# Kernel optimization log

Measured on AMD Instinct MI355X. Metric: run time of the kernel, lower is better.

Reference implementation:

```python
import jax, jax.numpy as jnp
import numpy as np

N = 16                      # input_dim (state dimension)
EPS = 1e-6
TRIL_R, TRIL_C = np.tril_indices(N)   # 136 lower-triangular slots


def setup_inputs() -> dict:
    key = jax.random.key(0)
    ks = jax.random.split(key, 7)
    B = 131072
    def xavier(k, fan_in, fan_out):
        lim = float(np.sqrt(6.0 / (fan_in + fan_out)))
        return jax.random.uniform(k, (fan_in, fan_out), jnp.float32, -lim, lim)
    return {
        "points": jax.random.normal(ks[0], (B, N), jnp.float32),
        "W0": xavier(ks[1], N, 512),
        "b0": jax.random.normal(ks[2], (512,), jnp.float32) * 0.01,
        "W1": xavier(ks[3], 512, 512),
        "b1": jax.random.normal(ks[4], (512,), jnp.float32) * 0.01,
        "W2": xavier(ks[5], 512, 136),
        "b2": jax.random.normal(ks[6], (136,), jnp.float32) * 0.01,
    }


def reference(points, W0, b0, W1, b1, W2, b2):
    # MLP: tanh, tanh, identity
    h = jnp.tanh(points @ W0 + b0)
    h = jnp.tanh(h @ W1 + b1)
    net = h @ W2 + b2                         # [B, 136] tril entries
    B = points.shape[0]
    # Batched scatter into lower-triangular matrices M: [B, N, N]
    M = jnp.zeros((B, N, N), points.dtype).at[:, TRIL_R, TRIL_C].set(net)
    # x^T (M M^T) x == ||M^T x||^2
    y = jnp.einsum('bij,bi->bj', M, points)   # (M^T x)_j = sum_i M_ij x_i
    vals = jnp.sum(y * y, axis=-1) + EPS * jnp.sum(points * points, axis=-1)
    return vals.reshape(-1, 1)
```

## Files before the change

### kernel.cpp

```cpp
#include <hip/hip_runtime.h>

typedef __bf16 bf16x4 __attribute__((ext_vector_type(4)));
typedef __bf16 bf16x8 __attribute__((ext_vector_type(8)));
typedef float f32x16 __attribute__((ext_vector_type(16)));

#define W0F_OFF 0
#define W1F_OFF 8192
#define W2F_OFF (8192 + 262144)
#define PREP_TOTAL (8192 + 262144 + 81920)

__global__ void prep_weights(const float* __restrict__ W0,
                             const float* __restrict__ W1,
                             const float* __restrict__ W2,
                             __bf16* __restrict__ ws) {
    int t = blockIdx.x * 256 + threadIdx.x;
    if (t < 8192) {
        int j = t & 7, lane = (t >> 3) & 63, nt = t >> 9;
        int n = nt * 32 + (lane & 31);
        int k = (lane >> 5) * 8 + j;
        ws[W0F_OFF + t] = (__bf16)W0[k * 512 + n];
    } else if (t < 8192 + 262144) {
        int u = t - 8192;
        int j = u & 7, lane = (u >> 3) & 63;
        int x = u >> 9;
        int kk = x & 31, nt = x >> 5;
        int n = nt * 32 + (lane & 31);
        int k = kk * 16 + (lane >> 5) * 8 + j;
        ws[W1F_OFF + u] = (__bf16)W1[k * 512 + n];
    } else if (t < PREP_TOTAL) {
        int v = t - (8192 + 262144);
        int j = v & 7, lane = (v >> 3) & 63;
        int x = v >> 9;
        int kk = x & 31, nt = x >> 5;
        int n = nt * 32 + (lane & 31);
        int k = kk * 16 + (lane >> 5) * 8 + j;
        ws[W2F_OFF + v] = (n < 136) ? (__bf16)W2[k * 136 + n] : (__bf16)0.0f;
    }
}

__device__ __forceinline__ float fast_tanh(float x) {
#if __has_builtin(__builtin_amdgcn_exp2f)
    float e = __builtin_amdgcn_exp2f(x * 2.885390081777926f);
#else
    float e = exp2f(x * 2.885390081777926f);
#endif
    return 1.0f - 2.0f * __builtin_amdgcn_rcpf(e + 1.0f);
}

#define HSTR 520
#define NSTR 140

__global__ __launch_bounds__(512, 2)
void fused_mlp_quad(const float* __restrict__ points,
                    const float* __restrict__ b0,
                    const float* __restrict__ b1,
                    const float* __restrict__ b2,
                    const __bf16* __restrict__ ws,
                    float* __restrict__ out) {
    __shared__ __align__(16) unsigned char lds_raw[66560];
    __bf16* h  = (__bf16*)lds_raw;
    float* net = (float*)lds_raw;

    const __bf16* w0f = ws + W0F_OFF;
    const __bf16* w1f = ws + W1F_OFF;
    const __bf16* w2f = ws + W2F_OFF;

    const int tid = threadIdx.x;
    const int w   = tid >> 6;
    const int l   = tid & 63;
    const int ln  = l & 31;
    const int hi  = l >> 5;
    const int row0 = blockIdx.x * 64;

    const int lofs = l * 8;
    const int ofs16 = (blockIdx.x >> 3) & 15;
    const int ofs8  = (blockIdx.x >> 3) & 7;

    {
        bf16x8 bx[2];
#pragma unroll
        for (int bt = 0; bt < 2; ++bt) {
            const float* src = points + (row0 + bt * 32 + ln) * 16 + hi * 8;
            float4 p0 = ((const float4*)src)[0];
            float4 p1 = ((const float4*)src)[1];
            bf16x8 v;
            v[0] = (__bf16)p0.x; v[1] = (__bf16)p0.y; v[2] = (__bf16)p0.z; v[3] = (__bf16)p0.w;
            v[4] = (__bf16)p1.x; v[5] = (__bf16)p1.y; v[6] = (__bf16)p1.z; v[7] = (__bf16)p1.w;
            bx[bt] = v;
        }
#pragma unroll
        for (int t = 0; t < 2; ++t) {
            const int ntg = w * 2 + t;
            bf16x8 wf = *(const bf16x8*)(w0f + ntg * 512 + lofs);
#pragma unroll
            for (int bt = 0; bt < 2; ++bt) {
                f32x16 acc = {};
                acc = __builtin_amdgcn_mfma_f32_32x32x16_bf16(wf, bx[bt], acc, 0, 0, 0);
#pragma unroll
                for (int rg = 0; rg < 4; ++rg) {
                    const int n0 = ntg * 32 + 8 * rg + 4 * hi;
                    float4 bias = *(const float4*)(b0 + n0);
                    bf16x4 v;
                    v[0] = (__bf16)fast_tanh(acc[4 * rg + 0] + bias.x);
                    v[1] = (__bf16)fast_tanh(acc[4 * rg + 1] + bias.y);
                    v[2] = (__bf16)fast_tanh(acc[4 * rg + 2] + bias.z);
                    v[3] = (__bf16)fast_tanh(acc[4 * rg + 3] + bias.w);
                    *(bf16x4*)(h + (bt * 32 + ln) * HSTR + n0) = v;
                }
            }
        }
    }
    __syncthreads();

    f32x16 acc1[2][2] = {};
    {
        const __bf16* arow0 = h + ln * HSTR + hi * 8;
        const __bf16* arow1 = h + (32 + ln) * HSTR + hi * 8;
        const __bf16* wb0 = w1f + (w * 2 + 0) * 16384 + lofs;
        const __bf16* wb1 = w1f + (w * 2 + 1) * 16384 + lofs;
        for (int ks2 = 0; ks2 < 16; ++ks2) {
            const int ks = (ks2 + ofs16) & 15;
            bf16x8 aa[2][2], bb[2][2];
#pragma unroll
            for (int u = 0; u < 2; ++u) {
                const int kk = ks * 2 + u;
                const int vo = kk * 512;
                aa[u][0] = *(const bf16x8*)(arow0 + kk * 16);
                aa[u][1] = *(const bf16x8*)(arow1 + kk * 16);
                bb[u][0] = *(const bf16x8*)(wb0 + vo);
                bb[u][1] = *(const bf16x8*)(wb1 + vo);
            }
#pragma unroll
            for (int u = 0; u < 2; ++u) {
#pragma unroll
                for (int t = 0; t < 2; ++t) {
                    acc1[0][t] = __builtin_amdgcn_mfma_f32_32x32x16_bf16(bb[u][t], aa[u][0], acc1[0][t], 0, 0, 0);
                    acc1[1][t] = __builtin_amdgcn_mfma_f32_32x32x16_bf16(bb[u][t], aa[u][1], acc1[1][t], 0, 0, 0);
                }
            }
        }
    }
    __syncthreads();
#pragma unroll
    for (int t = 0; t < 2; ++t) {
#pragma unroll
        for (int bt = 0; bt < 2; ++bt) {
#pragma unroll
            for (int rg = 0; rg < 4; ++rg) {
                const int n0 = (w * 2 + t) * 32 + 8 * rg + 4 * hi;
                float4 bias = *(const float4*)(b1 + n0);
                bf16x4 v;
                v[0] = (__bf16)fast_tanh(acc1[bt][t][4 * rg + 0] + bias.x);
                v[1] = (__bf16)fast_tanh(acc1[bt][t][4 * rg + 1] + bias.y);
                v[2] = (__bf16)fast_tanh(acc1[bt][t][4 * rg + 2] + bias.z);
                v[3] = (__bf16)fast_tanh(acc1[bt][t][4 * rg + 3] + bias.w);
                *(bf16x4*)(h + (bt * 32 + ln) * HSTR + n0) = v;
            }
        }
    }
    __syncthreads();

    f32x16 acc2a = {}, acc2e = {};
    const int nt2 = w >> 1;
    const int bt2 = w & 1;
    const bool two = (w < 2);
    {
        const __bf16* arowA = h + (bt2 * 32 + ln) * HSTR + hi * 8;
        const __bf16* arowE = h + ((w & 1) * 32 + ln) * HSTR + hi * 8;
        const __bf16* wbA = w2f + nt2 * 16384 + lofs;
        const __bf16* wbE = w2f + 4 * 16384 + lofs;
        for (int ks2 = 0; ks2 < 8; ++ks2) {
            const int ks = (ks2 + ofs8) & 7;
            bf16x8 aaA[2], wA[2], aaE[2], wE[2];
#pragma unroll
            for (int u = 0; u < 2; ++u) {
                const int kk = ks * 4 + u * 2;
                const int vo = kk * 512;
                aaA[u] = *(const bf16x8*)(arowA + kk * 16);
                wA[u]  = *(const bf16x8*)(wbA + vo);
                if (two) {
                    aaE[u] = *(const bf16x8*)(arowE + kk * 16);
                    wE[u]  = *(const bf16x8*)(wbE + vo);
                }
            }
            bf16x8 aaA2[2], wA2[2], aaE2[2], wE2[2];
#pragma unroll
            for (int u = 0; u < 2; ++u) {
                const int kk = ks * 4 + u * 2 + 1;
                const int vo = kk * 512;
                aaA2[u] = *(const bf16x8*)(arowA + kk * 16);
                wA2[u]  = *(const bf16x8*)(wbA + vo);
                if (two) {
                    aaE2[u] = *(const bf16x8*)(arowE + kk * 16);
                    wE2[u]  = *(const bf16x8*)(wbE + vo);
                }
            }
#pragma unroll
            for (int u = 0; u < 2; ++u) {
                acc2a = __builtin_amdgcn_mfma_f32_32x32x16_bf16(wA[u], aaA[u], acc2a, 0, 0, 0);
                acc2a = __builtin_amdgcn_mfma_f32_32x32x16_bf16(wA2[u], aaA2[u], acc2a, 0, 0, 0);
                if (two) {
                    acc2e = __builtin_amdgcn_mfma_f32_32x32x16_bf16(wE[u], aaE[u], acc2e, 0, 0, 0);
                    acc2e = __builtin_amdgcn_mfma_f32_32x32x16_bf16(wE2[u], aaE2[u], acc2e, 0, 0, 0);
                }
            }
        }
    }
    __syncthreads();
    {
#pragma unroll
        for (int rg = 0; rg < 4; ++rg) {
            const int n0 = nt2 * 32 + 8 * rg + 4 * hi;
            float4 bias = *(const float4*)(b2 + n0);
            float4 v;
            v.x = acc2a[4 * rg + 0] + bias.x;
            v.y = acc2a[4 * rg + 1] + bias.y;
            v.z = acc2a[4 * rg + 2] + bias.z;
            v.w = acc2a[4 * rg + 3] + bias.w;
            *(float4*)(net + (bt2 * 32 + ln) * NSTR + n0) = v;
        }
        if (two) {
            const int n0 = 128 + 4 * hi;
            float4 bias = *(const float4*)(b2 + n0);
            float4 v;
            v.x = acc2e[0] + bias.x;
            v.y = acc2e[1] + bias.y;
            v.z = acc2e[2] + bias.z;
            v.w = acc2e[3] + bias.w;
            *(float4*)(net + ((w & 1) * 32 + ln) * NSTR + n0) = v;
        }
    }
    __syncthreads();

    {
        const int r  = tid >> 3;
        const int jg = tid & 7;
        const float* xp = points + (row0 + r) * 16;
        float xv[16];
#pragma unroll
        for (int i = 0; i < 4; ++i) {
            float4 v = ((const float4*)xp)[i];
            xv[i * 4 + 0] = v.x; xv[i * 4 + 1] = v.y;
            xv[i * 4 + 2] = v.z; xv[i * 4 + 3] = v.w;
        }
        float sumsq = 0.f;
#pragma unroll
        for (int i = 0; i < 16; ++i) sumsq += xv[i] * xv[i];
        float p = 0.f;
#pragma unroll
        for (int jj = 0; jj < 2; ++jj) {
            const int j = jg + jj * 8;
            float y = 0.f;
#pragma unroll
            for (int i = 0; i < 16; ++i) {
                float mv = net[r * NSTR + ((i * (i + 1)) >> 1) + j];
                y += (i >= j) ? mv * xv[i] : 0.f;
            }
            p += y * y;
        }
        p += __shfl_xor(p, 1);
        p += __shfl_xor(p, 2);
        p += __shfl_xor(p, 4);
        if (jg == 0) out[row0 + r] = p + 1e-6f * sumsq;
    }
}

extern "C" void kernel_launch(void* const* d_in, const int* in_sizes, int n_in,
                              void* d_out, int out_size, void* d_ws, size_t ws_size,
                              hipStream_t stream) {
    const float* points = (const float*)d_in[0];
    const float* W0 = (const float*)d_in[1];
    const float* b0 = (const float*)d_in[2];
    const float* W1 = (const float*)d_in[3];
    const float* b1 = (const float*)d_in[4];
    const float* W2 = (const float*)d_in[5];
    const float* b2 = (const float*)d_in[6];
    __bf16* ws = (__bf16*)d_ws;
    float* out = (float*)d_out;

    prep_weights<<<(PREP_TOTAL + 255) / 256, 256, 0, stream>>>(W0, W1, W2, ws);

    const int B = in_sizes[0] / 16;
    fused_mlp_quad<<<B / 64, 512, 0, stream>>>(points, b0, b1, b2, ws, out);
}
```

Before: 188.5 us.

## Fold tanh scale into weights, vectorize weight prep, stagger first-wave blocks

Pre-multiplies W0 and W1 by the tanh exp2 constant during weight conversion, so each tanh drops one multiply (bias is folded with an fma). The prep kernel is rewritten so one wave writes a contiguous 512-element fragment as 16-byte vector stores. The first 512 blocks also sleep for a hash-based random delay so they do not all hit the same memory at once. The staggering adds idle time, and scaling before the bf16 cast changes rounding slightly.

Result: slower. 196.8 us (+4.4%).

```diff
diff --git a/kernel.cpp b/kernel.cpp
--- a/kernel.cpp
+++ b/kernel.cpp
@@ -4,45 +4,37 @@
 typedef __bf16 bf16x8 __attribute__((ext_vector_type(8)));
 typedef float f32x16 __attribute__((ext_vector_type(16)));
 
+#define TC 2.885390081777926f
+
 #define W0F_OFF 0
 #define W1F_OFF 8192
 #define W2F_OFF (8192 + 262144)
-#define PREP_TOTAL (8192 + 262144 + 81920)
 
 __global__ void prep_weights(const float* __restrict__ W0,
                              const float* __restrict__ W1,
                              const float* __restrict__ W2,
                              __bf16* __restrict__ ws) {
-    int t = blockIdx.x * 256 + threadIdx.x;
-    if (t < 8192) {
-        int j = t & 7, lane = (t >> 3) & 63, nt = t >> 9;
-        int n = nt * 32 + (lane & 31);
-        int k = (lane >> 5) * 8 + j;
-        ws[W0F_OFF + t] = (__bf16)W0[k * 512 + n];
-    } else if (t < 8192 + 262144) {
-        int u = t - 8192;
-        int j = u & 7, lane = (u >> 3) & 63;
-        int x = u >> 9;
-        int kk = x & 31, nt = x >> 5;
-        int n = nt * 32 + (lane & 31);
-        int k = kk * 16 + (lane >> 5) * 8 + j;
-        ws[W1F_OFF + u] = (__bf16)W1[k * 512 + n];
-    } else if (t < PREP_TOTAL) {
-        int v = t - (8192 + 262144);
-        int j = v & 7, lane = (v >> 3) & 63;
-        int x = v >> 9;
-        int kk = x & 31, nt = x >> 5;
-        int n = nt * 32 + (lane & 31);
-        int k = kk * 16 + (lane >> 5) * 8 + j;
-        ws[W2F_OFF + v] = (n < 136) ? (__bf16)W2[k * 136 + n] : (__bf16)0.0f;
-    }
-}
-
-__device__ __forceinline__ float fast_tanh(float x) {
+    const int wave = blockIdx.x * 8 + (threadIdx.x >> 6);
+    const int l   = threadIdx.x & 63;
+    const int col = l & 31, kh = l >> 5;
+    const float* src; int nt, kk, S, nlim; float scl;
+    if (wave < 16)       { src = W0; nt = wave; kk = 0;      S = 512; nlim = 512; scl = TC; }
+    else if (wave < 528) { int r = wave - 16;  src = W1; nt = r >> 5; kk = r & 31; S = 512; nlim = 512; scl = TC; }
+    else                 { int r = wave - 528; src = W2; nt = r >> 5; kk = r & 31; S = 136; nlim = 136; scl = 1.0f; }
+    const int n  = nt * 32 + col;
+    const int k0 = kk * 16 + kh * 8;
+    bf16x8 v;
+#pragma unroll
+    for (int j = 0; j < 8; ++j)
+        v[j] = (n < nlim) ? (__bf16)(src[(k0 + j) * S + n] * scl) : (__bf16)0.0f;
+    *(bf16x8*)(ws + wave * 512 + l * 8) = v;
+}
+
+__device__ __forceinline__ float fast_tanh_pre(float y) {
 #if __has_builtin(__builtin_amdgcn_exp2f)
-    float e = __builtin_amdgcn_exp2f(x * 2.885390081777926f);
+    float e = __builtin_amdgcn_exp2f(y);
 #else
-    float e = exp2f(x * 2.885390081777926f);
+    float e = exp2f(y);
 #endif
     return 1.0f - 2.0f * __builtin_amdgcn_rcpf(e + 1.0f);
 }
@@ -61,6 +53,18 @@
     __bf16* h  = (__bf16*)lds_raw;
     float* net = (float*)lds_raw;
 
+    {
+        const unsigned d = (blockIdx.x < 512)
+                         ? ((blockIdx.x * 2654435761u) >> 29) : 0u;
+        if (d > 0) __builtin_amdgcn_s_sleep(64);
+        if (d > 1) __builtin_amdgcn_s_sleep(64);
+        if (d > 2) __builtin_amdgcn_s_sleep(64);
+        if (d > 3) __builtin_amdgcn_s_sleep(64);
+        if (d > 4) __builtin_amdgcn_s_sleep(64);
+        if (d > 5) __builtin_amdgcn_s_sleep(64);
+        if (d > 6) __builtin_amdgcn_s_sleep(64);
+    }
+
     const __bf16* w0f = ws + W0F_OFF;
     const __bf16* w1f = ws + W1F_OFF;
     const __bf16* w2f = ws + W2F_OFF;
@@ -101,10 +105,10 @@
                     const int n0 = ntg * 32 + 8 * rg + 4 * hi;
                     float4 bias = *(const float4*)(b0 + n0);
                     bf16x4 v;
-                    v[0] = (__bf16)fast_tanh(acc[4 * rg + 0] + bias.x);
-                    v[1] = (__bf16)fast_tanh(acc[4 * rg + 1] + bias.y);
-                    v[2] = (__bf16)fast_tanh(acc[4 * rg + 2] + bias.z);
-                    v[3] = (__bf16)fast_tanh(acc[4 * rg + 3] + bias.w);
+                    v[0] = (__bf16)fast_tanh_pre(fmaf(TC, bias.x, acc[4 * rg + 0]));
+                    v[1] = (__bf16)fast_tanh_pre(fmaf(TC, bias.y, acc[4 * rg + 1]));
+                    v[2] = (__bf16)fast_tanh_pre(fmaf(TC, bias.z, acc[4 * rg + 2]));
+                    v[3] = (__bf16)fast_tanh_pre(fmaf(TC, bias.w, acc[4 * rg + 3]));
                     *(bf16x4*)(h + (bt * 32 + ln) * HSTR + n0) = v;
                 }
             }
@@ -150,10 +154,10 @@
                 const int n0 = (w * 2 + t) * 32 + 8 * rg + 4 * hi;
                 float4 bias = *(const float4*)(b1 + n0);
                 bf16x4 v;
-                v[0] = (__bf16)fast_tanh(acc1[bt][t][4 * rg + 0] + bias.x);
-                v[1] = (__bf16)fast_tanh(acc1[bt][t][4 * rg + 1] + bias.y);
-                v[2] = (__bf16)fast_tanh(acc1[bt][t][4 * rg + 2] + bias.z);
-                v[3] = (__bf16)fast_tanh(acc1[bt][t][4 * rg + 3] + bias.w);
+                v[0] = (__bf16)fast_tanh_pre(fmaf(TC, bias.x, acc1[bt][t][4 * rg + 0]));
+                v[1] = (__bf16)fast_tanh_pre(fmaf(TC, bias.y, acc1[bt][t][4 * rg + 1]));
+                v[2] = (__bf16)fast_tanh_pre(fmaf(TC, bias.z, acc1[bt][t][4 * rg + 2]));
+                v[3] = (__bf16)fast_tanh_pre(fmaf(TC, bias.w, acc1[bt][t][4 * rg + 3]));
                 *(bf16x4*)(h + (bt * 32 + ln) * HSTR + n0) = v;
             }
         }
@@ -278,7 +282,7 @@
     __bf16* ws = (__bf16*)d_ws;
     float* out = (float*)d_out;
 
-    prep_weights<<<(PREP_TOTAL + 255) / 256, 256, 0, stream>>>(W0, W1, W2, ws);
+    prep_weights<<<86, 512, 0, stream>>>(W0, W1, W2, ws);
 
     const int B = in_sizes[0] / 16;
     fused_mlp_quad<<<B / 64, 512, 0, stream>>>(points, b0, b1, b2, ws, out);
```
